# Performance work log

Measured on AMD Instinct MI355X. Metric: run time of the kernel, lower is better.

The kernel has to match this reference:

```python
import jax, jax.numpy as jnp
import numpy as np

# conv_ada hyperparameters from init_kwargs: ka=1, alpha=0.25, kw=0.2
KA1 = 1.0          # activation scale for conv1 (ka)
KA2 = 1.25         # activation scale for conv2 (ka + alpha)
KW = 0.2           # weight clipping threshold used by the binary weight STE


def ste_sign(x, clip=1.0):
    """Binary sign with straight-through estimator (hardtanh-style clip).
    Forward value is sign(x); gradient is that of clip(x, -clip, clip)."""
    xc = jnp.clip(x, -clip, clip)
    return xc + jax.lax.stop_gradient(jnp.sign(x) - xc)


def conv_bin(x, w, ka, kw):
    """1-bit activation / 1-bit weight 3x3 conv (conv_ada).
    Activations -> ka * sign(x); weights -> per-out-channel mean(|w|) * sign(w)."""
    xq = ka * ste_sign(x)
    alpha_w = jnp.mean(jnp.abs(w), axis=(1, 2, 3), keepdims=True)  # [O,1,1,1]
    wq = alpha_w * ste_sign(w, kw)
    return jax.lax.conv_general_dilated(
        xq, wq, window_strides=(1, 1), padding='SAME',
        dimension_numbers=('NCHW', 'OIHW', 'NCHW'))


def prelu(x, slope):
    # per-channel PReLU, slope shape [C]
    return jnp.where(x >= 0, x, slope[None, :, None, None] * x)


def pixel_shuffle(x, r=2):
    b, c, h, w = x.shape
    co = c // (r * r)
    x = x.reshape(b, co, r, r, h, w)
    x = x.transpose(0, 1, 4, 2, 5, 3)  # b, co, h, r, w, r
    return x.reshape(b, co, h * r, w * r)


def setup_inputs() -> dict:
    key = jax.random.key(0)
    ks = jax.random.split(key, 11)
    B, C, H, W = 8, 64, 256, 256
    return {
        'x': jax.random.normal(ks[0], (B, C, H, W), jnp.float32),
        'w1': jax.random.normal(ks[1], (C, C, 3, 3), jnp.float32) * 0.1,
        'w2': jax.random.normal(ks[2], (2 * C, C, 3, 3), jnp.float32) * 0.1,
        'b_in': jax.random.normal(ks[3], (1, C, 1, 1), jnp.float32) * 0.01,
        'b1': jax.random.normal(ks[4], (1, C, 1, 1), jnp.float32) * 0.01,
        's1': jax.random.uniform(ks[5], (C,), jnp.float32) * 0.25,
        'b2': jax.random.normal(ks[6], (1, C, 1, 1), jnp.float32) * 0.01,
        'b2_': jax.random.normal(ks[7], (1, C, 1, 1), jnp.float32) * 0.01,
        'b3': jax.random.normal(ks[8], (1, 2 * C, 1, 1), jnp.float32) * 0.01,
        's2': jax.random.uniform(ks[9], (2 * C,), jnp.float32) * 0.25,
        'b4': jax.random.normal(ks[10], (1, 2 * C, 1, 1), jnp.float32) * 0.01,
    }


def reference(x, w1, w2, b_in, b1, s1, b2, b2_, b3, s2, b4):
    out = conv_bin(x + b_in, w1, KA1, KW)       # move1_ -> conv1
    xres = out + x                              # residual x = out + x
    # NOTE: in the original forward, move1 -> prelu1 -> move2 are computed on
    # `out` and then immediately overwritten by out = move2_(x); that branch
    # is dead code and does not affect the output (b1, s1, b2 get zero grads).
    out = conv_bin(xres + b2_, w2, KA2, KW)     # move2_ -> conv2
    out = out + jnp.concatenate([xres, xres], axis=1)  # shortcut = cat(x, x)
    out = prelu(out + b3, s2) + b4              # move3 -> prelu2 -> move4
    return pixel_shuffle(out, 2)                # [B, C/2, 2H, 2W]
```

## Files before the change

kernel.cpp:

```cpp
#include <hip/hip_runtime.h>
#include <hip/hip_bf16.h>

typedef unsigned long long u64;
typedef unsigned int u32;
typedef unsigned short ushort8 __attribute__((ext_vector_type(8)));
typedef u64 u64x2 __attribute__((ext_vector_type(2)));
typedef float fx2 __attribute__((ext_vector_type(2)));

#define IMG_H 256
#define IMG_W 256
#define CIN   64
#define HW    (IMG_H * IMG_W)
#define NPIX  (8 * HW)

static __device__ __forceinline__ float bf16bits_to_f32(unsigned short h) {
    union { u32 u; float f; } c;
    c.u = ((u32)h) << 16;
    return c.f;
}
static __device__ __forceinline__ unsigned short f32_to_bf16bits(float f) {
    __hip_bfloat16 hb = __float2bfloat16(f);
    return *(unsigned short*)&hb;
}

__global__ void prep_kernel(const float* __restrict__ w1,
                            const float* __restrict__ w2,
                            u64* __restrict__ w1b, float* __restrict__ a1,
                            u64* __restrict__ w2b, float* __restrict__ a2) {
    int blk = blockIdx.x;
    int lane = threadIdx.x;
    const float* w;
    u64* wb;
    float* al;
    if (blk < 64) { w = w1 + (size_t)blk * 576;        wb = w1b + blk * 9;        al = a1 + blk; }
    else          { w = w2 + (size_t)(blk - 64) * 576; wb = w2b + (blk - 64) * 9; al = a2 + (blk - 64); }

    const float* wi = w + lane * 9;
    float s = 0.f;
    u64 bits[9];
#pragma unroll
    for (int t = 0; t < 9; ++t) {
        float v = wi[t];
        s += fabsf(v);
        bits[t] = __ballot(v > 0.f);
    }
#pragma unroll
    for (int m = 32; m >= 1; m >>= 1) s += __shfl_xor(s, m);
    if (lane == 0) {
        *al = s * (1.f / 576.f);
#pragma unroll
        for (int t = 0; t < 9; ++t) wb[t] = bits[t];
    }
}

__global__ __launch_bounds__(256)
void pack_kernel(const float* __restrict__ x,
                 const float* __restrict__ b_in,
                 u64* __restrict__ bits1) {
    int tid = blockIdx.x * 256 + threadIdx.x;
    int n = tid >> 15;
    int p = (tid & 32767) * 2;
    const float* xp = x + (size_t)n * CIN * HW + p;
    u32 w0lo = 0, w0hi = 0, w1lo = 0, w1hi = 0;
#pragma unroll
    for (int c = 0; c < 32; ++c) {
        fx2 v = *(const fx2*)(xp + (size_t)c * HW);
        float b = b_in[c];
        w0lo |= (u32)((v.x + b) > 0.f) << c;
        w1lo |= (u32)((v.y + b) > 0.f) << c;
    }
#pragma unroll
    for (int c = 0; c < 32; ++c) {
        fx2 v = *(const fx2*)(xp + (size_t)(c + 32) * HW);
        float b = b_in[c + 32];
        w0hi |= (u32)((v.x + b) > 0.f) << c;
        w1hi |= (u32)((v.y + b) > 0.f) << c;
    }
    u64x2 pk;
    pk.x = ((u64)w0hi << 32) | w0lo;
    pk.y = ((u64)w1hi << 32) | w1lo;
    *(u64x2*)(bits1 + (size_t)n * HW + p) = pk;
}

__global__ __launch_bounds__(256)
void conv1_kernel(const float* __restrict__ x,
                  const float* __restrict__ b2_,
                  const u64* __restrict__ bits1,
                  const u64* __restrict__ wbits,
                  const float* __restrict__ alpha1,
                  ushort8* __restrict__ xres,
                  u64* __restrict__ bits2) {
    int i = blockIdx.x * 256 + threadIdx.x;
    int n = i >> 16, p = i & 65535;
    int y = p >> 8, xc = p & 255;

    u64 xb[9];
    int invmask = 0, nv = 0;
#pragma unroll
    for (int t = 0; t < 9; ++t) {
        int dy = t / 3 - 1, dx = t % 3 - 1;
        bool v = ((unsigned)(y + dy) < (unsigned)IMG_H) &
                 ((unsigned)(xc + dx) < (unsigned)IMG_W);
        xb[t] = v ? bits1[i + dy * IMG_W + dx] : 0ull;
        invmask |= (v ? 0 : 1) << t;
        nv += v ? 1 : 0;
    }

    const float* xp = x + (size_t)n * CIN * HW + p;
    u64 w2 = 0;

#pragma unroll 2
    for (int g = 0; g < 8; ++g) {
        float rv[8];
#pragma unroll
        for (int j = 0; j < 8; ++j)
            rv[j] = xp[(size_t)(g * 8 + j) * HW];

        ushort8 pk;
        u32 gm = 0;
#pragma unroll
        for (int j = 0; j < 8; ++j) {
            int o = g * 8 + j;
            const u64* wo = wbits + o * 9;
            int D = 0;
#pragma unroll
            for (int t = 0; t < 9; ++t) D += __popcll(xb[t] ^ wo[t]);
            int S = 64 * nv - 2 * D;
            if (invmask) {
#pragma unroll
                for (int t = 0; t < 9; ++t)
                    if ((invmask >> t) & 1) S += 2 * __popcll(wo[t]);
            }
            float r = alpha1[o] * (float)S + rv[j];
            pk[j] = f32_to_bf16bits(r);
            gm |= (u32)((r + b2_[o]) > 0.f) << j;
        }
        xres[(size_t)(n * 8 + g) * HW + p] = pk;
        w2 |= (u64)gm << (8 * g);
    }
    bits2[i] = w2;
}

__global__ __launch_bounds__(256)
void conv2_kernel(const ushort8* __restrict__ xres,
                  const u64* __restrict__ bits2,
                  const u64* __restrict__ wbits,
                  const float* __restrict__ alpha2,
                  const float* __restrict__ b3,
                  const float* __restrict__ s2,
                  const float* __restrict__ b4,
                  float* __restrict__ out) {
    int i = blockIdx.x * 256 + threadIdx.x;
    int n = i >> 16, p = i & 65535;
    int y = p >> 8, xc = p & 255;

    u64 xb[9];
    int invmask = 0, nv = 0;
#pragma unroll
    for (int t = 0; t < 9; ++t) {
        int dy = t / 3 - 1, dx = t % 3 - 1;
        bool v = ((unsigned)(y + dy) < (unsigned)IMG_H) &
                 ((unsigned)(xc + dx) < (unsigned)IMG_W);
        xb[t] = v ? bits2[i + dy * IMG_W + dx] : 0ull;
        invmask |= (v ? 0 : 1) << t;
        nv += v ? 1 : 0;
    }

    float* ob = out + (size_t)n * 32 * 512 * 512;
    const int Y = 2 * y, X = 2 * xc;

#pragma unroll 2
    for (int g = 0; g < 8; ++g) {
        ushort8 xr = xres[(size_t)(n * 8 + g) * HW + p];
        float vlo[8], vhi[8];
#pragma unroll
        for (int j = 0; j < 8; ++j) {
            int o = g * 8 + j;
            float xrv = bf16bits_to_f32(xr[j]);
            {
                const u64* wo = wbits + o * 9;
                int D = 0;
#pragma unroll
                for (int t = 0; t < 9; ++t) D += __popcll(xb[t] ^ wo[t]);
                int S = 64 * nv - 2 * D;
                if (invmask) {
#pragma unroll
                    for (int t = 0; t < 9; ++t)
                        if ((invmask >> t) & 1) S += 2 * __popcll(wo[t]);
                }
                float u = 1.25f * alpha2[o] * (float)S + xrv + b3[o];
                u = (u >= 0.f) ? u : s2[o] * u;
                vlo[j] = u + b4[o];
            }
            {
                int o2 = o + 64;
                const u64* wo = wbits + o2 * 9;
                int D = 0;
#pragma unroll
                for (int t = 0; t < 9; ++t) D += __popcll(xb[t] ^ wo[t]);
                int S = 64 * nv - 2 * D;
                if (invmask) {
#pragma unroll
                    for (int t = 0; t < 9; ++t)
                        if ((invmask >> t) & 1) S += 2 * __popcll(wo[t]);
                }
                float u = 1.25f * alpha2[o2] * (float)S + xrv + b3[o2];
                u = (u >= 0.f) ? u : s2[o2] * u;
                vhi[j] = u + b4[o2];
            }
        }
#pragma unroll
        for (int jj = 0; jj < 8; jj += 2) {
            int o = g * 8 + jj;
            int co = o >> 2;
            int r1 = (o >> 1) & 1;
            fx2 vl; vl.x = vlo[jj]; vl.y = vlo[jj + 1];
            fx2 vh; vh.x = vhi[jj]; vh.y = vhi[jj + 1];
            __builtin_nontemporal_store(
                vl, (fx2*)(ob + ((size_t)co * 512 + Y + r1) * 512 + X));
            __builtin_nontemporal_store(
                vh, (fx2*)(ob + ((size_t)(co + 16) * 512 + Y + r1) * 512 + X));
        }
    }
}

extern "C" void kernel_launch(void* const* d_in, const int* in_sizes, int n_in,
                              void* d_out, int out_size, void* d_ws, size_t ws_size,
                              hipStream_t stream) {
    const float* x    = (const float*)d_in[0];
    const float* w1   = (const float*)d_in[1];
    const float* w2   = (const float*)d_in[2];
    const float* b_in = (const float*)d_in[3];
    const float* b2_  = (const float*)d_in[7];
    const float* b3   = (const float*)d_in[8];
    const float* s2   = (const float*)d_in[9];
    const float* b4   = (const float*)d_in[10];
    float* out = (float*)d_out;

    char* ws = (char*)d_ws;
    u64*   w1b   = (u64*)(ws + 0);
    u64*   w2b   = (u64*)(ws + 4608);
    float* a1    = (float*)(ws + 13824);
    float* a2    = (float*)(ws + 14080);
    u64*   bits1 = (u64*)(ws + 16384);
    u64*   bits2 = (u64*)(ws + 16384 + 4194304);
    ushort8* xres = (ushort8*)(ws + 16384 + 2 * 4194304);

    prep_kernel<<<192, 64, 0, stream>>>(w1, w2, w1b, a1, w2b, a2);

    pack_kernel <<<NPIX / 512, 256, 0, stream>>>(x, b_in, bits1);
    conv1_kernel<<<NPIX / 256, 256, 0, stream>>>(x, b2_, bits1, w1b, a1, xres, bits2);
    conv2_kernel<<<NPIX / 256, 256, 0, stream>>>(xres, bits2, w2b, a2, b3, s2, b4, out);
}
```

Baseline: 218.7 us.

## Fuse pack, conv1 and conv2 into one tiled kernel with shared-memory halos

Replaces the three per-pixel kernels with a single kernel that processes 32x16 pixel tiles. Each tile binarizes x into shared memory with a 2-pixel halo, computes conv1 and the residual in registers, and recomputes conv1 on the 1-pixel halo ring so conv2 can read its bit inputs from shared memory. This removes the global round-trips for bits1, bits2 and the bf16 xres buffer, which also drops the bf16 rounding of the residual. In exchange the halo is recomputed redundantly by a few threads, which diverges, each thread holds 64 floats in registers, and 512-thread blocks may lower occupancy.

Result: slower. 443.0 us (+102.5%).

```diff
diff --git a/kernel.cpp b/kernel.cpp
--- a/kernel.cpp
+++ b/kernel.cpp
@@ -3,25 +3,13 @@
 
 typedef unsigned long long u64;
 typedef unsigned int u32;
-typedef unsigned short ushort8 __attribute__((ext_vector_type(8)));
-typedef u64 u64x2 __attribute__((ext_vector_type(2)));
 typedef float fx2 __attribute__((ext_vector_type(2)));
 
 #define IMG_H 256
 #define IMG_W 256
 #define CIN   64
 #define HW    (IMG_H * IMG_W)
-#define NPIX  (8 * HW)
-
-static __device__ __forceinline__ float bf16bits_to_f32(unsigned short h) {
-    union { u32 u; float f; } c;
-    c.u = ((u32)h) << 16;
-    return c.f;
-}
-static __device__ __forceinline__ unsigned short f32_to_bf16bits(float f) {
-    __hip_bfloat16 hb = __float2bfloat16(f);
-    return *(unsigned short*)&hb;
-}
+
 
 __global__ void prep_kernel(const float* __restrict__ w1,
                             const float* __restrict__ w2,
@@ -53,169 +41,219 @@
     }
 }
 
-__global__ __launch_bounds__(256)
-void pack_kernel(const float* __restrict__ x,
-                 const float* __restrict__ b_in,
-                 u64* __restrict__ bits1) {
-    int tid = blockIdx.x * 256 + threadIdx.x;
-    int n = tid >> 15;
-    int p = (tid & 32767) * 2;
-    const float* xp = x + (size_t)n * CIN * HW + p;
-    u32 w0lo = 0, w0hi = 0, w1lo = 0, w1hi = 0;
-#pragma unroll
-    for (int c = 0; c < 32; ++c) {
-        fx2 v = *(const fx2*)(xp + (size_t)c * HW);
-        float b = b_in[c];
-        w0lo |= (u32)((v.x + b) > 0.f) << c;
-        w1lo |= (u32)((v.y + b) > 0.f) << c;
-    }
-#pragma unroll
-    for (int c = 0; c < 32; ++c) {
-        fx2 v = *(const fx2*)(xp + (size_t)(c + 32) * HW);
-        float b = b_in[c + 32];
-        w0hi |= (u32)((v.x + b) > 0.f) << c;
-        w1hi |= (u32)((v.y + b) > 0.f) << c;
-    }
-    u64x2 pk;
-    pk.x = ((u64)w0hi << 32) | w0lo;
-    pk.y = ((u64)w1hi << 32) | w1lo;
-    *(u64x2*)(bits1 + (size_t)n * HW + p) = pk;
-}
-
-__global__ __launch_bounds__(256)
-void conv1_kernel(const float* __restrict__ x,
+__global__ __launch_bounds__(512)
+void fused_kernel(const float* __restrict__ x,
+                  const float* __restrict__ b_in,
                   const float* __restrict__ b2_,
-                  const u64* __restrict__ bits1,
-                  const u64* __restrict__ wbits,
+                  const u64* __restrict__ w1bits,
                   const float* __restrict__ alpha1,
-                  ushort8* __restrict__ xres,
-                  u64* __restrict__ bits2) {
-    int i = blockIdx.x * 256 + threadIdx.x;
-    int n = i >> 16, p = i & 65535;
-    int y = p >> 8, xc = p & 255;
-
-    u64 xb[9];
-    int invmask = 0, nv = 0;
-#pragma unroll
-    for (int t = 0; t < 9; ++t) {
-        int dy = t / 3 - 1, dx = t % 3 - 1;
-        bool v = ((unsigned)(y + dy) < (unsigned)IMG_H) &
-                 ((unsigned)(xc + dx) < (unsigned)IMG_W);
-        xb[t] = v ? bits1[i + dy * IMG_W + dx] : 0ull;
-        invmask |= (v ? 0 : 1) << t;
-        nv += v ? 1 : 0;
-    }
-
-    const float* xp = x + (size_t)n * CIN * HW + p;
-    u64 w2 = 0;
-
-#pragma unroll 2
-    for (int g = 0; g < 8; ++g) {
-        float rv[8];
-#pragma unroll
-        for (int j = 0; j < 8; ++j)
-            rv[j] = xp[(size_t)(g * 8 + j) * HW];
-
-        ushort8 pk;
-        u32 gm = 0;
-#pragma unroll
-        for (int j = 0; j < 8; ++j) {
-            int o = g * 8 + j;
-            const u64* wo = wbits + o * 9;
-            int D = 0;
-#pragma unroll
-            for (int t = 0; t < 9; ++t) D += __popcll(xb[t] ^ wo[t]);
-            int S = 64 * nv - 2 * D;
-            if (invmask) {
-#pragma unroll
-                for (int t = 0; t < 9; ++t)
-                    if ((invmask >> t) & 1) S += 2 * __popcll(wo[t]);
-            }
-            float r = alpha1[o] * (float)S + rv[j];
-            pk[j] = f32_to_bf16bits(r);
-            gm |= (u32)((r + b2_[o]) > 0.f) << j;
-        }
-        xres[(size_t)(n * 8 + g) * HW + p] = pk;
-        w2 |= (u64)gm << (8 * g);
-    }
-    bits2[i] = w2;
-}
-
-__global__ __launch_bounds__(256)
-void conv2_kernel(const ushort8* __restrict__ xres,
-                  const u64* __restrict__ bits2,
-                  const u64* __restrict__ wbits,
+                  const u64* __restrict__ w2bits,
                   const float* __restrict__ alpha2,
                   const float* __restrict__ b3,
                   const float* __restrict__ s2,
                   const float* __restrict__ b4,
                   float* __restrict__ out) {
-    int i = blockIdx.x * 256 + threadIdx.x;
-    int n = i >> 16, p = i & 65535;
-    int y = p >> 8, xc = p & 255;
-
-    u64 xb[9];
-    int invmask = 0, nv = 0;
+    __shared__ u64 b1[20][36];
+    __shared__ u64 b2[18][34];
+
+    const int tid = threadIdx.x;
+    const int n = blockIdx.z;
+    const int tx0 = blockIdx.x * 32;
+    const int ty0 = blockIdx.y * 16;
+    const float* xn = x + (size_t)n * CIN * HW;
+
+    const int py = tid >> 5;
+    const int lx = tid & 31;
+    const int gy = ty0 + py, gx = tx0 + lx;
+    const int p = gy * IMG_W + gx;
+
+    float rv[64];
+    {
+        u32 blo = 0, bhi = 0;
+#pragma unroll
+        for (int c = 0; c < 32; ++c) {
+            float v = xn[(size_t)c * HW + p];
+            rv[c] = v;
+            blo |= (u32)((v + b_in[c]) > 0.f) << c;
+        }
+#pragma unroll
+        for (int c = 0; c < 32; ++c) {
+            float v = xn[(size_t)(c + 32) * HW + p];
+            rv[c + 32] = v;
+            bhi |= (u32)((v + b_in[c + 32]) > 0.f) << c;
+        }
+        b1[py + 2][lx + 2] = ((u64)bhi << 32) | blo;
+    }
+
+    if (tid < 208) {
+        int wy, wx;
+        if (tid < 72)       { wy = tid / 36;            wx = tid % 36; }
+        else if (tid < 144) { wy = 18 + (tid - 72) / 36; wx = (tid - 72) % 36; }
+        else {
+            int r = tid - 144;
+            wy = 2 + (r >> 2);
+            int c4 = r & 3;
+            wx = (c4 < 2) ? c4 : c4 + 32;
+        }
+        int ggy = ty0 + wy - 2, ggx = tx0 + wx - 2;
+        u64 w = 0;
+        if ((unsigned)ggy < (unsigned)IMG_H && (unsigned)ggx < (unsigned)IMG_W) {
+            const float* pp = xn + ggy * IMG_W + ggx;
+            u32 lo = 0, hi = 0;
+#pragma unroll
+            for (int c = 0; c < 32; ++c)
+                lo |= (u32)((pp[(size_t)c * HW] + b_in[c]) > 0.f) << c;
+#pragma unroll
+            for (int c = 0; c < 32; ++c)
+                hi |= (u32)((pp[(size_t)(c + 32) * HW] + b_in[c + 32]) > 0.f) << c;
+            w = ((u64)hi << 32) | lo;
+        }
+        b1[wy][wx] = w;
+    }
+    __syncthreads();
+
+    int invm = 0, nv = 0;
 #pragma unroll
     for (int t = 0; t < 9; ++t) {
         int dy = t / 3 - 1, dx = t % 3 - 1;
-        bool v = ((unsigned)(y + dy) < (unsigned)IMG_H) &
-                 ((unsigned)(xc + dx) < (unsigned)IMG_W);
-        xb[t] = v ? bits2[i + dy * IMG_W + dx] : 0ull;
-        invmask |= (v ? 0 : 1) << t;
+        bool v = ((unsigned)(gy + dy) < (unsigned)IMG_H) &
+                 ((unsigned)(gx + dx) < (unsigned)IMG_W);
+        invm |= (v ? 0 : 1) << t;
         nv += v ? 1 : 0;
     }
 
+    {
+        u64 W1[9];
+#pragma unroll
+        for (int t = 0; t < 9; ++t)
+            W1[t] = b1[py + 1 + t / 3][lx + 1 + t % 3];
+
+        u64 w2own = 0;
+#pragma unroll
+        for (int g = 0; g < 8; ++g) {
+            u32 gm = 0;
+#pragma unroll
+            for (int j = 0; j < 8; ++j) {
+                int o = g * 8 + j;
+                const u64* wo = w1bits + o * 9;
+                int D = 0;
+#pragma unroll
+                for (int t = 0; t < 9; ++t) D += __popcll(W1[t] ^ wo[t]);
+                int S = 64 * nv - 2 * D;
+                if (invm) {
+#pragma unroll
+                    for (int t = 0; t < 9; ++t)
+                        if ((invm >> t) & 1) S += 2 * __popcll(wo[t]);
+                }
+                float r = alpha1[o] * (float)S + rv[o];
+                rv[o] = r;
+                gm |= (u32)((r + b2_[o]) > 0.f) << j;
+            }
+            w2own |= (u64)gm << (8 * g);
+        }
+        b2[py + 1][lx + 1] = w2own;
+    }
+
+    if (tid < 100) {
+        int fy, fx;
+        if (tid < 34)      { fy = 0;  fx = tid; }
+        else if (tid < 68) { fy = 17; fx = tid - 34; }
+        else { int r = tid - 68; fy = 1 + (r >> 1); fx = (r & 1) ? 33 : 0; }
+        int ggy = ty0 + fy - 1, ggx = tx0 + fx - 1;
+        u64 w2w = 0;
+        if ((unsigned)ggy < (unsigned)IMG_H && (unsigned)ggx < (unsigned)IMG_W) {
+            u64 xb[9];
+            int im = 0, nvv = 0;
+#pragma unroll
+            for (int t = 0; t < 9; ++t) {
+                int dy = t / 3 - 1, dx = t % 3 - 1;
+                bool v = ((unsigned)(ggy + dy) < (unsigned)IMG_H) &
+                         ((unsigned)(ggx + dx) < (unsigned)IMG_W);
+                xb[t] = b1[fy + t / 3][fx + t % 3];
+                im |= (v ? 0 : 1) << t;
+                nvv += v ? 1 : 0;
+            }
+            const float* pp = xn + ggy * IMG_W + ggx;
+#pragma unroll
+            for (int g = 0; g < 8; ++g) {
+                u32 gm = 0;
+#pragma unroll
+                for (int j = 0; j < 8; ++j) {
+                    int o = g * 8 + j;
+                    const u64* wo = w1bits + o * 9;
+                    int D = 0;
+#pragma unroll
+                    for (int t = 0; t < 9; ++t) D += __popcll(xb[t] ^ wo[t]);
+                    int S = 64 * nvv - 2 * D;
+                    if (im) {
+#pragma unroll
+                        for (int t = 0; t < 9; ++t)
+                            if ((im >> t) & 1) S += 2 * __popcll(wo[t]);
+                    }
+                    float r = alpha1[o] * (float)S + pp[(size_t)o * HW];
+                    gm |= (u32)((r + b2_[o]) > 0.f) << j;
+                }
+                w2w |= (u64)gm << (8 * g);
+            }
+        }
+        b2[fy][fx] = w2w;
+    }
+    __syncthreads();
+
+    u64 W2[9];
+#pragma unroll
+    for (int t = 0; t < 9; ++t)
+        W2[t] = b2[py + t / 3][lx + t % 3];
+
     float* ob = out + (size_t)n * 32 * 512 * 512;
-    const int Y = 2 * y, X = 2 * xc;
-
-#pragma unroll 2
+    const int Y = 2 * gy, X = 2 * gx;
+
+#pragma unroll
     for (int g = 0; g < 8; ++g) {
-        ushort8 xr = xres[(size_t)(n * 8 + g) * HW + p];
-        float vlo[8], vhi[8];
-#pragma unroll
-        for (int j = 0; j < 8; ++j) {
-            int o = g * 8 + j;
-            float xrv = bf16bits_to_f32(xr[j]);
-            {
-                const u64* wo = wbits + o * 9;
-                int D = 0;
-#pragma unroll
-                for (int t = 0; t < 9; ++t) D += __popcll(xb[t] ^ wo[t]);
-                int S = 64 * nv - 2 * D;
-                if (invmask) {
-#pragma unroll
-                    for (int t = 0; t < 9; ++t)
-                        if ((invmask >> t) & 1) S += 2 * __popcll(wo[t]);
-                }
-                float u = 1.25f * alpha2[o] * (float)S + xrv + b3[o];
-                u = (u >= 0.f) ? u : s2[o] * u;
-                vlo[j] = u + b4[o];
-            }
-            {
-                int o2 = o + 64;
-                const u64* wo = wbits + o2 * 9;
-                int D = 0;
-#pragma unroll
-                for (int t = 0; t < 9; ++t) D += __popcll(xb[t] ^ wo[t]);
-                int S = 64 * nv - 2 * D;
-                if (invmask) {
-#pragma unroll
-                    for (int t = 0; t < 9; ++t)
-                        if ((invmask >> t) & 1) S += 2 * __popcll(wo[t]);
-                }
-                float u = 1.25f * alpha2[o2] * (float)S + xrv + b3[o2];
-                u = (u >= 0.f) ? u : s2[o2] * u;
-                vhi[j] = u + b4[o2];
-            }
-        }
 #pragma unroll
         for (int jj = 0; jj < 8; jj += 2) {
+            float vlo[2], vhi[2];
+#pragma unroll
+            for (int q = 0; q < 2; ++q) {
+                int o = g * 8 + jj + q;
+                float xrv = rv[o];
+                {
+                    const u64* wo = w2bits + o * 9;
+                    int D = 0;
+#pragma unroll
+                    for (int t = 0; t < 9; ++t) D += __popcll(W2[t] ^ wo[t]);
+                    int S = 64 * nv - 2 * D;
+                    if (invm) {
+#pragma unroll
+                        for (int t = 0; t < 9; ++t)
+                            if ((invm >> t) & 1) S += 2 * __popcll(wo[t]);
+                    }
+                    float u = 1.25f * alpha2[o] * (float)S + xrv + b3[o];
+                    u = (u >= 0.f) ? u : s2[o] * u;
+                    vlo[q] = u + b4[o];
+                }
+                {
+                    int o2 = o + 64;
+                    const u64* wo = w2bits + o2 * 9;
+                    int D = 0;
+#pragma unroll
+                    for (int t = 0; t < 9; ++t) D += __popcll(W2[t] ^ wo[t]);
+                    int S = 64 * nv - 2 * D;
+                    if (invm) {
+#pragma unroll
+                        for (int t = 0; t < 9; ++t)
+                            if ((invm >> t) & 1) S += 2 * __popcll(wo[t]);
+                    }
+                    float u = 1.25f * alpha2[o2] * (float)S + xrv + b3[o2];
+                    u = (u >= 0.f) ? u : s2[o2] * u;
+                    vhi[q] = u + b4[o2];
+                }
+            }
             int o = g * 8 + jj;
             int co = o >> 2;
             int r1 = (o >> 1) & 1;
-            fx2 vl; vl.x = vlo[jj]; vl.y = vlo[jj + 1];
-            fx2 vh; vh.x = vhi[jj]; vh.y = vhi[jj + 1];
+            fx2 vl; vl.x = vlo[0]; vl.y = vlo[1];
+            fx2 vh; vh.x = vhi[0]; vh.y = vhi[1];
             __builtin_nontemporal_store(
                 vl, (fx2*)(ob + ((size_t)co * 512 + Y + r1) * 512 + X));
             __builtin_nontemporal_store(
@@ -238,17 +276,14 @@
     float* out = (float*)d_out;
 
     char* ws = (char*)d_ws;
-    u64*   w1b   = (u64*)(ws + 0);
-    u64*   w2b   = (u64*)(ws + 4608);
-    float* a1    = (float*)(ws + 13824);
-    float* a2    = (float*)(ws + 14080);
-    u64*   bits1 = (u64*)(ws + 16384);
-    u64*   bits2 = (u64*)(ws + 16384 + 4194304);
-    ushort8* xres = (ushort8*)(ws + 16384 + 2 * 4194304);
+    u64*   w1b = (u64*)(ws + 0);
+    u64*   w2b = (u64*)(ws + 4608);
+    float* a1  = (float*)(ws + 13824);
+    float* a2  = (float*)(ws + 14080);
 
     prep_kernel<<<192, 64, 0, stream>>>(w1, w2, w1b, a1, w2b, a2);
 
-    pack_kernel <<<NPIX / 512, 256, 0, stream>>>(x, b_in, bits1);
-    conv1_kernel<<<NPIX / 256, 256, 0, stream>>>(x, b2_, bits1, w1b, a1, xres, bits2);
-    conv2_kernel<<<NPIX / 256, 256, 0, stream>>>(xres, bits2, w2b, a2, b3, s2, b4, out);
+    dim3 grid(IMG_W / 32, IMG_H / 16, 8);
+    fused_kernel<<<grid, 512, 0, stream>>>(x, b_in, b2_, w1b, a1, w2b, a2,
+                                           b3, s2, b4, out);
 }
```
